# Kernel tuning notes

Measured on AMD Instinct MI355X. Metric: run time of the kernel, lower is better.

The kernel has to match this reference:

```python
import jax, jax.numpy as jnp
import numpy as np

D = 1024; DI = 2048; DS = 16; DTR = 64; K = 4          # mamba dims
HR = 16; DHR = 64                                       # rwkv heads
HA = 32; DHA = 32                                       # attention heads
NM = 6; NR = 4; NT = 2                                  # layer counts
B = 2; L = 1024


def _rms(x, w):
    return x * jax.lax.rsqrt(jnp.mean(x * x, axis=-1, keepdims=True) + 1e-6) * w


def _dwconv(x, w, b):
    # causal depthwise conv over seq; x [B,L,DI], w [K,1,DI]
    xp = jnp.pad(x, ((0, 0), (K - 1, 0), (0, 0)))
    y = jax.lax.conv_general_dilated(xp, w, (1,), 'VALID',
        dimension_numbers=('NWC', 'WIO', 'NWC'), feature_group_count=DI)
    return y + b


def _selective_scan(u, delta, A, Bm, Cm):
    # u,delta [B,L,DI]; A [DI,DS]; Bm,Cm [B,L,DS]
    def step(h, inp):
        u_t, d_t, b_t, c_t = inp
        dA = jnp.exp(d_t[:, :, None] * A)                     # [B,DI,DS]
        h = h * dA + (d_t * u_t)[:, :, None] * b_t[:, None, :]
        return h, jnp.einsum('bds,bs->bd', h, c_t)
    h0 = jnp.zeros((u.shape[0], DI, DS), u.dtype)
    tm = lambda a: jnp.swapaxes(a, 0, 1)                      # time-major
    _, ys = jax.lax.scan(step, h0, (tm(u), tm(delta), tm(Bm), tm(Cm)))
    return jnp.swapaxes(ys, 0, 1)


def _mamba(x, p):
    norm, Win, cw, cb, Wx, Wdt, bdt, Alog, Dp, Wout = p
    xn = _rms(x, norm)
    xz = xn @ Win                                             # [B,L,2*DI]
    xc, z = jnp.split(xz, 2, axis=-1)
    xc = jax.nn.silu(_dwconv(xc, cw, cb))
    xdbl = xc @ Wx                                            # [B,L,DTR+2*DS]
    dt = xdbl[..., :DTR]
    Bm = xdbl[..., DTR:DTR + DS]
    Cm = xdbl[..., DTR + DS:]
    delta = jax.nn.softplus(dt @ Wdt + bdt)                   # [B,L,DI]
    A = -jnp.exp(Alog)
    y = _selective_scan(xc, delta, A, Bm, Cm) + Dp * xc
    y = y * jax.nn.silu(z)
    return x + y @ Wout


def _rwkv(x, p):
    norm, mu, Wr, Wk, Wv, Wo, wlog, u = p
    Bb, Ll = x.shape[0], x.shape[1]
    xn = _rms(x, norm)
    xs = jnp.pad(xn, ((0, 0), (1, 0), (0, 0)))[:, :-1, :]     # token shift
    mix = lambda m: xn * m + xs * (1.0 - m)
    r = (mix(mu[0]) @ Wr).reshape(Bb, Ll, HR, DHR)
    k = (mix(mu[1]) @ Wk).reshape(Bb, Ll, HR, DHR)
    v = (mix(mu[2]) @ Wv).reshape(Bb, Ll, HR, DHR)
    w = jnp.exp(-jnp.exp(wlog))                               # decay in (0,1)
    def step(S, inp):
        r_t, k_t, v_t = inp                                   # [B,HR,DHR]
        kv = jnp.einsum('bhk,bhv->bhkv', k_t, v_t)
        y = jnp.einsum('bhk,bhkv->bhv', r_t, S + u[None, :, :, None] * kv)
        return w[None, :, :, None] * S + kv, y
    S0 = jnp.zeros((Bb, HR, DHR, DHR), x.dtype)
    tm = lambda a: jnp.swapaxes(a, 0, 1)
    _, ys = jax.lax.scan(step, S0, (tm(r), tm(k), tm(v)))
    y = jnp.swapaxes(ys, 0, 1).reshape(Bb, Ll, D)
    return x + y @ Wo


def _mha(x, p):
    Wq, bq, Wk, bk, Wv, bv, Wo, bo = p
    q = jnp.einsum('bld,dhk->blhk', x, Wq) + bq
    k = jnp.einsum('bld,dhk->blhk', x, Wk) + bk
    v = jnp.einsum('bld,dhk->blhk', x, Wv) + bv
    scale = 1.0 / float(np.sqrt(DHA))
    att = jax.nn.softmax(jnp.einsum('blhk,bmhk->bhlm', q, k) * scale, axis=-1)
    o = jnp.einsum('bhlm,bmhk->blhk', att, v)
    return jnp.einsum('blhk,hkd->bld', o, Wo) + bo


def setup_inputs() -> dict:
    key = jax.random.key(0)
    ks = iter(jax.random.split(key, 40))
    nrm = lambda s, sc=0.02: jax.random.normal(next(ks), s, jnp.float32) * sc
    return {
        'x': jax.random.normal(next(ks), (B, L, D), jnp.float32),
        'm_norm': jnp.ones((NM, D), jnp.float32),
        'm_Win': nrm((NM, D, 2 * DI)),
        'm_conv_w': nrm((NM, K, 1, DI)),
        'm_conv_b': jnp.zeros((NM, DI), jnp.float32),
        'm_Wx': nrm((NM, DI, DTR + 2 * DS)),
        'm_Wdt': nrm((NM, DTR, DI)),
        'm_bdt': jnp.full((NM, DI), -4.6, jnp.float32),
        'm_Alog': jnp.broadcast_to(jnp.log(jnp.arange(1, DS + 1, dtype=jnp.float32)), (NM, DI, DS)) + jnp.zeros((NM, DI, DS), jnp.float32),
        'm_D': jnp.ones((NM, DI), jnp.float32),
        'm_Wout': nrm((NM, DI, D)),
        'r_norm': jnp.ones((NR, D), jnp.float32),
        'r_mu': jax.random.uniform(next(ks), (NR, 3, D), jnp.float32),
        'r_Wr': nrm((NR, D, D)), 'r_Wk': nrm((NR, D, D)),
        'r_Wv': nrm((NR, D, D)), 'r_Wo': nrm((NR, D, D)),
        'r_wlog': nrm((NR, HR, DHR), 0.5),
        'r_u': nrm((NR, HR, DHR), 0.5),
        'a_Wq': nrm((NT, D, HA, DHA)), 'a_bq': jnp.zeros((NT, HA, DHA), jnp.float32),
        'a_Wk': nrm((NT, D, HA, DHA)), 'a_bk': jnp.zeros((NT, HA, DHA), jnp.float32),
        'a_Wv': nrm((NT, D, HA, DHA)), 'a_bv': jnp.zeros((NT, HA, DHA), jnp.float32),
        'a_Wo': nrm((NT, HA, DHA, D)), 'a_bo': jnp.zeros((NT, D), jnp.float32),
        'f_W': nrm((3 * D, 3)), 'f_b': jnp.zeros((3,), jnp.float32),
    }


def reference(x, m_norm, m_Win, m_conv_w, m_conv_b, m_Wx, m_Wdt, m_bdt, m_Alog, m_D, m_Wout,
              r_norm, r_mu, r_Wr, r_Wk, r_Wv, r_Wo, r_wlog, r_u,
              a_Wq, a_bq, a_Wk, a_bk, a_Wv, a_bv, a_Wo, a_bo, f_W, f_b):
    m = x
    for i in range(NM):
        m = _mamba(m, (m_norm[i], m_Win[i], m_conv_w[i], m_conv_b[i], m_Wx[i],
                       m_Wdt[i], m_bdt[i], m_Alog[i], m_D[i], m_Wout[i]))
    r = x
    for i in range(NR):
        r = _rwkv(r, (r_norm[i], r_mu[i], r_Wr[i], r_Wk[i], r_Wv[i], r_Wo[i],
                      r_wlog[i], r_u[i]))
    t = x
    for i in range(NT):
        t = _mha(t, (a_Wq[i], a_bq[i], a_Wk[i], a_bk[i], a_Wv[i], a_bv[i],
                     a_Wo[i], a_bo[i]))
    combined = jnp.concatenate([m, r, t], axis=-1)           # [B,L,3*D]
    return jax.nn.softmax(combined @ f_W + f_b, axis=-1)     # [B,L,3]
```

## Files before the change

### kernel.cpp

```cpp
#include <hip/hip_runtime.h>
#include <hip/hip_bf16.h>
#include <cstddef>

#define D_   1024
#define DI_  2048
#define DS_  16
#define DTR_ 64
#define KC_  4
#define HR_  16
#define DHR_ 64
#define HA_  32
#define DHA_ 32
#define NM_  6
#define NR_  4
#define NT_  2
#define B_   2
#define L_   1024
#define NBL  (B_*L_)

typedef __hip_bfloat16 bf16;
typedef __attribute__((ext_vector_type(8))) short short8v;
typedef __attribute__((ext_vector_type(4))) float float4v;

__device__ __forceinline__ float bfbits2f(unsigned short u) {
    return __uint_as_float(((unsigned int)u) << 16);
}
__device__ __forceinline__ float b2f(bf16 x) { return __bfloat162float(x); }
__device__ __forceinline__ unsigned short f2bfbits(float f) {
    bf16 h = __float2bfloat16(f);
    return *reinterpret_cast<unsigned short*>(&h);
}
__device__ __forceinline__ float ldf(const void* p, long i, int bf) {
    if (bf) return bfbits2f(((const unsigned short*)p)[i]);
    return ((const float*)p)[i];
}
__device__ __forceinline__ float softplus_f(float x) {
    return x > 20.f ? x : log1pf(__expf(x));
}
__device__ __forceinline__ float silu_f(float x) {
    return x / (1.f + __expf(-x));
}

__global__ __launch_bounds__(256) void diag_k(float* __restrict__ out, float code)
{
    const int idx = blockIdx.x * 256 + threadIdx.x;
    if (idx < NBL * 3) out[idx] = (idx == 0 ? code : 0.f);
}

__global__ __launch_bounds__(64) void detect_k(const void* __restrict__ x,
                                               int* __restrict__ flag)
{
    const unsigned short* u = (const unsigned short*)x;
    int local = 0;
    for (int i = threadIdx.x; i < 1024; i += 64) {
        const float av = fabsf(bfbits2f(u[i]));
        if (!(av < 1e6f)) local = 1;
    }
    const unsigned long long b = __ballot(local);
    if (threadIdx.x == 0) flag[0] = b ? 0 : 1;
}

#define BM 64
#define BN 64
#define TK 64
#define LDT 72

__global__ __launch_bounds__(256) void gemm_k(
    const void* __restrict__ A, int lda, int aDt,
    const void* __restrict__ W, long woff,
    const void* __restrict__ bias, long boff, int hasBias,
    void* __restrict__ C, int ldc, int cDt,
    int N, int K, int act, int acc,
    const int* __restrict__ flagp)
{
    const int bf = *flagp;
    __shared__ short As[BM * LDT];
    __shared__ short Bs[BN * LDT];
    const int bm = blockIdx.y * BM;
    const int bn = blockIdx.x * BN;
    const int tid = threadIdx.x;
    const int lane = tid & 63;
    const int wid = tid >> 6;
    const int wr = wid >> 1, wc = wid & 1;

    const int sa_row = tid >> 2;
    const int sa_kq  = (tid & 3) << 4;
    const int sb_col = tid & 63;
    const int sb_kq  = (tid >> 6) << 4;
    const int sb_gn  = bn + sb_col;

    float4v accv[2][2] = {};

    for (int k0 = 0; k0 < K; k0 += TK) {
        {
            short8v a0, a1;
            const size_t aoff = (size_t)(bm + sa_row) * lda + k0 + sa_kq;
            if (aDt) {
                a0 = *(const short8v*)((const unsigned short*)A + aoff);
                a1 = *(const short8v*)((const unsigned short*)A + aoff + 8);
            } else {
                const float* ap = (const float*)A + aoff;
                const float4 v0 = *(const float4*)(ap + 0);
                const float4 v1 = *(const float4*)(ap + 4);
                const float4 v2 = *(const float4*)(ap + 8);
                const float4 v3 = *(const float4*)(ap + 12);
                a0[0]=f2bfbits(v0.x); a0[1]=f2bfbits(v0.y); a0[2]=f2bfbits(v0.z); a0[3]=f2bfbits(v0.w);
                a0[4]=f2bfbits(v1.x); a0[5]=f2bfbits(v1.y); a0[6]=f2bfbits(v1.z); a0[7]=f2bfbits(v1.w);
                a1[0]=f2bfbits(v2.x); a1[1]=f2bfbits(v2.y); a1[2]=f2bfbits(v2.z); a1[3]=f2bfbits(v2.w);
                a1[4]=f2bfbits(v3.x); a1[5]=f2bfbits(v3.y); a1[6]=f2bfbits(v3.z); a1[7]=f2bfbits(v3.w);
            }
            *(short8v*)&As[sa_row * LDT + sa_kq + 0] = a0;
            *(short8v*)&As[sa_row * LDT + sa_kq + 8] = a1;
        }
        {
            short8v b0, b1;
            #pragma unroll
            for (int j = 0; j < 8; ++j) { b0[j] = 0; b1[j] = 0; }
            if (sb_gn < N) {
                const long wbase = woff + (long)(k0 + sb_kq) * N + sb_gn;
                if (bf) {
                    const unsigned short* wp = (const unsigned short*)W;
                    #pragma unroll
                    for (int j = 0; j < 8; ++j) {
                        b0[j] = (short)wp[wbase + (long)j * N];
                        b1[j] = (short)wp[wbase + (long)(j + 8) * N];
                    }
                } else {
                    const float* wp = (const float*)W;
                    #pragma unroll
                    for (int j = 0; j < 8; ++j) {
                        b0[j] = (short)f2bfbits(wp[wbase + (long)j * N]);
                        b1[j] = (short)f2bfbits(wp[wbase + (long)(j + 8) * N]);
                    }
                }
            }
            *(short8v*)&Bs[sb_col * LDT + sb_kq + 0] = b0;
            *(short8v*)&Bs[sb_col * LDT + sb_kq + 8] = b1;
        }
        __syncthreads();
        {
            const int r  = lane & 15;
            const int kb = (lane >> 4) << 3;
            #pragma unroll
            for (int ks = 0; ks < TK; ks += 32) {
                const int kg = ks + kb;
                const short8v a0 = *(const short8v*)&As[(wr*32 +      r) * LDT + kg];
                const short8v a1 = *(const short8v*)&As[(wr*32 + 16 + r) * LDT + kg];
                const short8v b0 = *(const short8v*)&Bs[(wc*32 +      r) * LDT + kg];
                const short8v b1 = *(const short8v*)&Bs[(wc*32 + 16 + r) * LDT + kg];
                accv[0][0] = __builtin_amdgcn_mfma_f32_16x16x32_bf16(a0, b0, accv[0][0], 0, 0, 0);
                accv[0][1] = __builtin_amdgcn_mfma_f32_16x16x32_bf16(a0, b1, accv[0][1], 0, 0, 0);
                accv[1][0] = __builtin_amdgcn_mfma_f32_16x16x32_bf16(a1, b0, accv[1][0], 0, 0, 0);
                accv[1][1] = __builtin_amdgcn_mfma_f32_16x16x32_bf16(a1, b1, accv[1][1], 0, 0, 0);
            }
        }
        __syncthreads();
    }

    const int crow0 = bm + wr * 32 + ((lane >> 4) << 2);
    const int ccol0 = bn + wc * 32 + (lane & 15);
    #pragma unroll
    for (int ni = 0; ni < 2; ++ni) {
        const int col = ccol0 + ni * 16;
        if (col < N) {
            const float bsv = hasBias ? ldf(bias, boff + col, bf) : 0.f;
            #pragma unroll
            for (int mi = 0; mi < 2; ++mi) {
                #pragma unroll
                for (int j = 0; j < 4; ++j) {
                    const int row = crow0 + mi * 16 + j;
                    float r = accv[mi][ni][j] + bsv;
                    if (act == 1) r = softplus_f(r);
                    if (cDt) {
                        ((bf16*)C)[(size_t)row * ldc + col] = __float2bfloat16(r);
                    } else {
                        float* cp = (float*)C + (size_t)row * ldc + col;
                        if (acc) r += *cp;
                        *cp = r;
                    }
                }
            }
        }
    }
}

__global__ __launch_bounds__(256) void cast3_k(const void* __restrict__ x,
    float* __restrict__ a, float* __restrict__ b, float* __restrict__ c,
    const int* __restrict__ flagp)
{
    const int bf = *flagp;
    const int idx = blockIdx.x * 256 + threadIdx.x;
    const float v = ldf(x, idx, bf);
    a[idx] = v; b[idx] = v; c[idx] = v;
}

__global__ __launch_bounds__(256) void rmsnorm_k(const float* __restrict__ x,
    const void* __restrict__ wgt, long woff, float* __restrict__ out,
    const int* __restrict__ flagp)
{
    const int bf = *flagp;
    const int row = blockIdx.x;
    const float* xr = x + (size_t)row * D_;
    float ss = 0.f;
    for (int i = threadIdx.x; i < D_; i += 256) { const float v = xr[i]; ss = fmaf(v, v, ss); }
    #pragma unroll
    for (int msk = 1; msk < 64; msk <<= 1) ss += __shfl_xor(ss, msk);
    __shared__ float red[4];
    if ((threadIdx.x & 63) == 0) red[threadIdx.x >> 6] = ss;
    __syncthreads();
    ss = red[0] + red[1] + red[2] + red[3];
    const float scale = rsqrtf(ss * (1.f / D_) + 1e-6f);
    float* orow = out + (size_t)row * D_;
    for (int i = threadIdx.x; i < D_; i += 256)
        orow[i] = xr[i] * scale * ldf(wgt, woff + i, bf);
}

__global__ __launch_bounds__(256) void conv_silu_k(const bf16* __restrict__ xz,
    const void* __restrict__ cw, long cwoff, const void* __restrict__ cb, long cboff,
    bf16* __restrict__ out, const int* __restrict__ flagp)
{
    const int bf = *flagp;
    const int idx = blockIdx.x * 256 + threadIdx.x;
    const int c = idx & (DI_ - 1);
    const int l = (idx >> 11) & (L_ - 1);
    const int b = idx >> 21;
    float acc = ldf(cb, cboff + c, bf);
    #pragma unroll
    for (int j = 0; j < KC_; ++j) {
        const int ls = l - (KC_ - 1) + j;
        if (ls >= 0)
            acc = fmaf(b2f(xz[((size_t)(b * L_ + ls)) * (2 * DI_) + c]),
                       ldf(cw, cwoff + j * DI_ + c, bf), acc);
    }
    out[idx] = __float2bfloat16(silu_f(acc));
}

#define MS_NCH 16
#define MS_CH  (L_ / MS_NCH)

__global__ __launch_bounds__(256) void mamba_scan_k(
    const bf16* __restrict__ u, const bf16* __restrict__ dlt,
    const float* __restrict__ xdbl, bf16* __restrict__ xz,
    const void* __restrict__ Alog, long aoff, const void* __restrict__ Dp, long doff,
    const int* __restrict__ flagp)
{
    const int bf = *flagp;
    const int bid = blockIdx.x;
    const int d = bid & (DI_ - 1);
    const int b = bid >> 11;
    const int s = threadIdx.x & (DS_ - 1);
    const int c = threadIdx.x >> 4;
    const float Av = -__expf(ldf(Alog, aoff + d * DS_ + s, bf));
    const float Dv = ldf(Dp, doff + d, bf);

    __shared__ float Pl[MS_NCH][DS_];
    __shared__ float Sl[MS_NCH][DS_];

    const int l0 = c * MS_CH;

    float P = 1.f, S = 0.f;
    for (int i = 0; i < MS_CH; ++i) {
        const size_t row = (size_t)(b * L_ + l0 + i);
        const float ut = b2f(u[row * DI_ + d]);
        const float dt = b2f(dlt[row * DI_ + d]);
        const float Bv = xdbl[row * 96 + 64 + s];
        const float dA = __expf(dt * Av);
        P *= dA;
        S = fmaf(S, dA, dt * ut * Bv);
    }
    Pl[c][s] = P; Sl[c][s] = S;
    __syncthreads();

    float hs = 0.f;
    for (int cc = 0; cc < c; ++cc) hs = fmaf(hs, Pl[cc][s], Sl[cc][s]);

    for (int i = 0; i < MS_CH; ++i) {
        const size_t row = (size_t)(b * L_ + l0 + i);
        const float ut = b2f(u[row * DI_ + d]);
        const float dt = b2f(dlt[row * DI_ + d]);
        const float Bv = xdbl[row * 96 + 64 + s];
        const float Cv = xdbl[row * 96 + 80 + s];
        const float dA = __expf(dt * Av);
        hs = fmaf(hs, dA, dt * ut * Bv);
        float yp = hs * Cv;
        yp += __shfl_xor(yp, 1, 16);
        yp += __shfl_xor(yp, 2, 16);
        yp += __shfl_xor(yp, 4, 16);
        yp += __shfl_xor(yp, 8, 16);
        if (s == 0) {
            const float z = b2f(xz[row * (2 * DI_) + DI_ + d]);
            xz[row * (2 * DI_) + d] = __float2bfloat16((yp + Dv * ut) * silu_f(z));
        }
    }
}

__global__ __launch_bounds__(256) void rwkv_mix_k(const float* __restrict__ xn,
    const void* __restrict__ mu, long muoff, bf16* __restrict__ o0,
    bf16* __restrict__ o1, bf16* __restrict__ o2, const int* __restrict__ flagp)
{
    const int bf = *flagp;
    const int idx = blockIdx.x * 256 + threadIdx.x;
    const int d = idx & (D_ - 1);
    const int l = (idx >> 10) & (L_ - 1);
    const float cur = xn[idx];
    const float prev = (l > 0) ? xn[idx - D_] : 0.f;
    const float m0 = ldf(mu, muoff + d, bf);
    const float m1 = ldf(mu, muoff + D_ + d, bf);
    const float m2 = ldf(mu, muoff + 2 * D_ + d, bf);
    o0[idx] = __float2bfloat16(cur * m0 + prev * (1.f - m0));
    o1[idx] = __float2bfloat16(cur * m1 + prev * (1.f - m1));
    o2[idx] = __float2bfloat16(cur * m2 + prev * (1.f - m2));
}

#define RW_NCH 16
#define RW_CH  (L_ / RW_NCH)

__global__ __launch_bounds__(1024) void rwkv_scan_k(const bf16* __restrict__ R,
    const bf16* __restrict__ Kb, const bf16* __restrict__ V,
    const void* __restrict__ wlog, long woff, const void* __restrict__ uu, long uoff,
    bf16* __restrict__ Y, const int* __restrict__ flagp)
{
    const int bf = *flagp;
    const int bid = blockIdx.x;
    const int v = bid & (DHR_ - 1);
    const int h = (bid >> 6) & (HR_ - 1);
    const int b = bid >> 10;
    const int k = threadIdx.x & 63;
    const int c = threadIdx.x >> 6;
    const float ew = __expf(ldf(wlog, woff + h * DHR_ + k, bf));
    const float w  = __expf(-ew);
    const float wC = __expf(-ew * (float)RW_CH);
    const float uv = ldf(uu, uoff + h * DHR_ + k, bf);

    __shared__ float Se[RW_NCH][64];

    const int l0 = c * RW_CH;

    float S = 0.f;
    for (int i = 0; i < RW_CH; ++i) {
        const size_t off = ((size_t)(b * L_ + l0 + i)) * D_ + h * DHR_;
        const float kk = b2f(Kb[off + k]);
        const float vt = b2f(V[off + v]);
        S = fmaf(w, S, kk * vt);
    }
    Se[c][k] = S;
    __syncthreads();

    S = 0.f;
    for (int cc = 0; cc < c; ++cc) S = fmaf(wC, S, Se[cc][k]);

    for (int i = 0; i < RW_CH; ++i) {
        const size_t off = ((size_t)(b * L_ + l0 + i)) * D_ + h * DHR_;
        const float r  = b2f(R[off + k]);
        const float kk = b2f(Kb[off + k]);
        const float vt = b2f(V[off + v]);
        const float kv = kk * vt;
        float yp = r * fmaf(uv, kv, S);
        S = fmaf(w, S, kv);
        yp += __shfl_xor(yp, 1);
        yp += __shfl_xor(yp, 2);
        yp += __shfl_xor(yp, 4);
        yp += __shfl_xor(yp, 8);
        yp += __shfl_xor(yp, 16);
        yp += __shfl_xor(yp, 32);
        if (k == 0) Y[off + v] = __float2bfloat16(yp);
    }
}

__global__ __launch_bounds__(256) void mha_attn_k(const bf16* __restrict__ Q,
    const bf16* __restrict__ Kx, const bf16* __restrict__ V, bf16* __restrict__ O)
{
    const int b = blockIdx.z, h = blockIdx.y;
    const int ql = blockIdx.x * 256 + threadIdx.x;
    __shared__ float Ks[32][33];
    __shared__ float Vs[32][33];
    float q[32], o[32];
    #pragma unroll
    for (int d = 0; d < 32; ++d) o[d] = 0.f;
    float mrun = -1e30f, lsum = 0.f;
    const size_t qoff = ((size_t)(b * L_ + ql)) * D_ + h * DHA_;
    #pragma unroll
    for (int d = 0; d < 32; ++d) q[d] = b2f(Q[qoff + d]) * 0.1767766952966369f;

    for (int kt = 0; kt < L_; kt += 32) {
        __syncthreads();
        {
            const int r = threadIdx.x >> 3;
            const int c = (threadIdx.x & 7) << 2;
            const size_t koff = ((size_t)(b * L_ + kt + r)) * D_ + h * DHA_ + c;
            const ushort4 k4 = *(const ushort4*)((const unsigned short*)Kx + koff);
            Ks[r][c + 0] = bfbits2f(k4.x); Ks[r][c + 1] = bfbits2f(k4.y);
            Ks[r][c + 2] = bfbits2f(k4.z); Ks[r][c + 3] = bfbits2f(k4.w);
            const ushort4 v4 = *(const ushort4*)((const unsigned short*)V + koff);
            Vs[r][c + 0] = bfbits2f(v4.x); Vs[r][c + 1] = bfbits2f(v4.y);
            Vs[r][c + 2] = bfbits2f(v4.z); Vs[r][c + 3] = bfbits2f(v4.w);
        }
        __syncthreads();
        for (int j = 0; j < 32; ++j) {
            float s = 0.f;
            #pragma unroll
            for (int d = 0; d < 32; ++d) s = fmaf(q[d], Ks[j][d], s);
            const float mn = fmaxf(mrun, s);
            const float corr = __expf(mrun - mn);
            const float p = __expf(s - mn);
            lsum = lsum * corr + p;
            #pragma unroll
            for (int d = 0; d < 32; ++d) o[d] = o[d] * corr + p * Vs[j][d];
            mrun = mn;
        }
    }
    const float inv = 1.f / lsum;
    #pragma unroll
    for (int d = 0; d < 32; ++d) O[qoff + d] = __float2bfloat16(o[d] * inv);
}

__global__ __launch_bounds__(256) void final_k(const float* __restrict__ m,
    const float* __restrict__ r, const float* __restrict__ t,
    const void* __restrict__ fW, const void* __restrict__ fb,
    float* __restrict__ out, const int* __restrict__ flagp)
{
    const int bf = *flagp;
    const int row = blockIdx.x;
    float p0 = 0.f, p1 = 0.f, p2 = 0.f;
    for (int i = threadIdx.x; i < 3 * D_; i += 256) {
        float v;
        if (i < D_)          v = m[(size_t)row * D_ + i];
        else if (i < 2 * D_) v = r[(size_t)row * D_ + i - D_];
        else                 v = t[(size_t)row * D_ + i - 2 * D_];
        p0 = fmaf(v, ldf(fW, (long)i * 3 + 0, bf), p0);
        p1 = fmaf(v, ldf(fW, (long)i * 3 + 1, bf), p1);
        p2 = fmaf(v, ldf(fW, (long)i * 3 + 2, bf), p2);
    }
    #pragma unroll
    for (int msk = 1; msk < 64; msk <<= 1) {
        p0 += __shfl_xor(p0, msk);
        p1 += __shfl_xor(p1, msk);
        p2 += __shfl_xor(p2, msk);
    }
    __shared__ float red[4][3];
    if ((threadIdx.x & 63) == 0) {
        const int w = threadIdx.x >> 6;
        red[w][0] = p0; red[w][1] = p1; red[w][2] = p2;
    }
    __syncthreads();
    if (threadIdx.x == 0) {
        const float l0 = red[0][0] + red[1][0] + red[2][0] + red[3][0] + ldf(fb, 0, bf);
        const float l1 = red[0][1] + red[1][1] + red[2][1] + red[3][1] + ldf(fb, 1, bf);
        const float l2 = red[0][2] + red[1][2] + red[2][2] + red[3][2] + ldf(fb, 2, bf);
        const float mx = fmaxf(l0, fmaxf(l1, l2));
        const float e0 = __expf(l0 - mx), e1 = __expf(l1 - mx), e2 = __expf(l2 - mx);
        const float inv = 1.f / (e0 + e1 + e2);
        out[row * 3 + 0] = e0 * inv;
        out[row * 3 + 1] = e1 * inv;
        out[row * 3 + 2] = e2 * inv;
    }
}

extern "C" void kernel_launch(void* const* d_in, const int* in_sizes, int n_in,
                              void* d_out, int out_size, void* d_ws, size_t ws_size,
                              hipStream_t stream)
{
    float* out = (float*)d_out;

    static const int expected[29] = {
        2097152, 6144, 25165824, 49152, 12288, 1179648, 786432, 12288,
        196608, 12288, 12582912, 4096, 12288, 4194304, 4194304, 4194304,
        4194304, 4096, 4096, 2097152, 2048, 2097152, 2048, 2097152, 2048,
        2097152, 2048, 9216, 3 };
    int bad = (n_in == 29) ? -1 : 29;
    if (bad < 0)
        for (int i = 0; i < 29; ++i)
            if (in_sizes[i] != expected[i]) { bad = i; break; }
    if (bad >= 0) {
        diag_k<<<24, 256, 0, stream>>>(out, 1000.f + 8.f * bad);
        return;
    }

    const size_t REQ = 64 + 3ull * 8388608 + 8388608 + 16777216 + 8388608 + 786432;
    if (ws_size < REQ) {
        diag_k<<<24, 256, 0, stream>>>(out, 2048.f + (float)(ws_size >> 20));
        return;
    }
    char* base = (char*)d_ws;
    int*   flag = (int*)base;
    float* resM = (float*)(base + 64);
    float* resR = resM + 2097152;
    float* resT = resR + 2097152;
    float* bufN = resT + 2097152;
    bf16*  XZ16 = (bf16*)(bufN + 2097152);
    bf16*  U16  = XZ16 + (size_t)NBL * 4096;
    float* XD   = (float*)(U16 + (size_t)NBL * 2048);

    bf16* q0 = XZ16;
    bf16* q1 = XZ16 + 1 * 2097152;
    bf16* q2 = XZ16 + 2 * 2097152;
    bf16* q3 = XZ16 + 3 * 2097152;
    bf16* u0 = U16;
    bf16* u1 = U16 + 2097152;

    const void* x        = d_in[0];
    const void* m_norm   = d_in[1];
    const void* m_Win    = d_in[2];
    const void* m_conv_w = d_in[3];
    const void* m_conv_b = d_in[4];
    const void* m_Wx     = d_in[5];
    const void* m_Wdt    = d_in[6];
    const void* m_bdt    = d_in[7];
    const void* m_Alog   = d_in[8];
    const void* m_D      = d_in[9];
    const void* m_Wout   = d_in[10];
    const void* r_norm   = d_in[11];
    const void* r_mu     = d_in[12];
    const void* r_Wr     = d_in[13];
    const void* r_Wk     = d_in[14];
    const void* r_Wv     = d_in[15];
    const void* r_Wo     = d_in[16];
    const void* r_wlog   = d_in[17];
    const void* r_u      = d_in[18];
    const void* a_Wq     = d_in[19];
    const void* a_bq     = d_in[20];
    const void* a_Wk     = d_in[21];
    const void* a_bk     = d_in[22];
    const void* a_Wv     = d_in[23];
    const void* a_bv     = d_in[24];
    const void* a_Wo     = d_in[25];
    const void* a_bo     = d_in[26];
    const void* f_W      = d_in[27];
    const void* f_b      = d_in[28];

    auto gemm = [&](const void* A, int lda, int aDt, const void* W, long woff,
                    const void* bias, long boff, int hasBias,
                    void* C, int ldc, int cDt, int N, int K, int act, int acc) {
        dim3 g((N + BN - 1) / BN, NBL / BM);
        gemm_k<<<g, 256, 0, stream>>>(A, lda, aDt, W, woff, bias, boff, hasBias,
                                      C, ldc, cDt, N, K, act, acc, flag);
    };

    detect_k<<<1, 64, 0, stream>>>(x, flag);
    cast3_k<<<8192, 256, 0, stream>>>(x, resM, resR, resT, flag);

    for (int i = 0; i < NM_; ++i) {
        rmsnorm_k<<<NBL, 256, 0, stream>>>(resM, m_norm, (long)i * D_, bufN, flag);
        gemm(bufN, D_, 0, m_Win, (long)i * D_ * 2 * DI_, nullptr, 0, 0,
             XZ16, 2 * DI_, 1, 2 * DI_, D_, 0, 0);
        conv_silu_k<<<16384, 256, 0, stream>>>(XZ16, m_conv_w, (long)i * KC_ * DI_,
                                               m_conv_b, (long)i * DI_, U16, flag);
        gemm(U16, DI_, 1, m_Wx, (long)i * DI_ * 96, nullptr, 0, 0,
             XD, 96, 0, 96, DI_, 0, 0);
        gemm(XD, 96, 0, m_Wdt, (long)i * DTR_ * DI_, m_bdt, (long)i * DI_, 1,
             bufN, DI_, 1, DI_, DTR_, 1 , 0);
        mamba_scan_k<<<B_ * DI_, 256, 0, stream>>>(U16, (const bf16*)bufN, XD, XZ16,
            m_Alog, (long)i * DI_ * DS_, m_D, (long)i * DI_, flag);
        gemm(XZ16, 2 * DI_, 1, m_Wout, (long)i * DI_ * D_, nullptr, 0, 0,
             resM, D_, 0, D_, DI_, 0, 1 );
    }

    for (int i = 0; i < NR_; ++i) {
        rmsnorm_k<<<NBL, 256, 0, stream>>>(resR, r_norm, (long)i * D_, bufN, flag);
        rwkv_mix_k<<<8192, 256, 0, stream>>>(bufN, r_mu, (long)i * 3 * D_,
                                             q0, q1, q2, flag);
        gemm(q0, D_, 1, r_Wr, (long)i * D_ * D_, nullptr, 0, 0, u0, D_, 1, D_, D_, 0, 0);
        gemm(q1, D_, 1, r_Wk, (long)i * D_ * D_, nullptr, 0, 0, u1, D_, 1, D_, D_, 0, 0);
        gemm(q2, D_, 1, r_Wv, (long)i * D_ * D_, nullptr, 0, 0, q3, D_, 1, D_, D_, 0, 0);
        rwkv_scan_k<<<B_ * HR_ * DHR_, RW_NCH * 64, 0, stream>>>(u0, u1, q3,
            r_wlog, (long)i * HR_ * DHR_, r_u, (long)i * HR_ * DHR_, q0, flag);
        gemm(q0, D_, 1, r_Wo, (long)i * D_ * D_, nullptr, 0, 0, resR, D_, 0, D_, D_, 0, 1);
    }

    for (int i = 0; i < NT_; ++i) {
        gemm(resT, D_, 0, a_Wq, (long)i * D_ * HA_ * DHA_, a_bq, (long)i * HA_ * DHA_, 1,
             u0, D_, 1, D_, D_, 0, 0);
        gemm(resT, D_, 0, a_Wk, (long)i * D_ * HA_ * DHA_, a_bk, (long)i * HA_ * DHA_, 1,
             u1, D_, 1, D_, D_, 0, 0);
        gemm(resT, D_, 0, a_Wv, (long)i * D_ * HA_ * DHA_, a_bv, (long)i * HA_ * DHA_, 1,
             q3, D_, 1, D_, D_, 0, 0);
        mha_attn_k<<<dim3(L_ / 256, HA_, B_), 256, 0, stream>>>(u0, u1, q3, q0);
        gemm(q0, D_, 1, a_Wo, (long)i * HA_ * DHA_ * D_, a_bo, (long)i * D_, 1,
             resT, D_, 0, D_, HA_ * DHA_, 0, 0 );
    }

    final_k<<<NBL, 256, 0, stream>>>(resM, resR, resT, f_W, f_b, out, flag);
}
```

Measured before the change: 4.958 ms.

## Rewrite MHA attention as flash-attention using bf16 MFMA tiles

Replaces the scalar per-thread online-softmax attention with a flash-attention style kernel. Each wave computes QK^T and PV for 16 queries using 16x16x32 bf16 MFMA instructions. K and V are staged as bf16 in LDS, with V transposed, and softmax probabilities go through a per-wave LDS buffer. The grid grows to 64 queries per block, which raises parallelism. Probabilities are rounded to bf16 before the PV product, which slightly changes numerics.

```diff
diff --git a/kernel.cpp b/kernel.cpp
--- a/kernel.cpp
+++ b/kernel.cpp
@@ -367,51 +367,99 @@
     }
 }
 
+#define LDK 40
+#define LDV 72
+
 __global__ __launch_bounds__(256) void mha_attn_k(const bf16* __restrict__ Q,
     const bf16* __restrict__ Kx, const bf16* __restrict__ V, bf16* __restrict__ O)
 {
     const int b = blockIdx.z, h = blockIdx.y;
-    const int ql = blockIdx.x * 256 + threadIdx.x;
-    __shared__ float Ks[32][33];
-    __shared__ float Vs[32][33];
-    float q[32], o[32];
-    #pragma unroll
-    for (int d = 0; d < 32; ++d) o[d] = 0.f;
-    float mrun = -1e30f, lsum = 0.f;
-    const size_t qoff = ((size_t)(b * L_ + ql)) * D_ + h * DHA_;
-    #pragma unroll
-    for (int d = 0; d < 32; ++d) q[d] = b2f(Q[qoff + d]) * 0.1767766952966369f;
-
-    for (int kt = 0; kt < L_; kt += 32) {
+    const int qt = blockIdx.x;
+    const int tid = threadIdx.x;
+    const int lane = tid & 63;
+    const int wid = tid >> 6;
+
+    __shared__ __align__(16) short Ks[64 * LDK];
+    __shared__ __align__(16) short Vt[32 * LDV];
+    __shared__ __align__(16) short Ps[4][16 * LDV];
+
+    const int fc  = lane & 15;
+    const int g   = lane >> 4;
+    const int fk8 = g << 3;
+
+    const int q0 = qt * 64 + wid * 16;
+
+    const size_t qoff = ((size_t)(b * L_ + q0 + fc)) * D_ + h * DHA_ + fk8;
+    const short8v qf = *(const short8v*)((const unsigned short*)Q + qoff);
+
+    float4v o0 = {}, o1 = {};
+    float m[4] = {-1e30f, -1e30f, -1e30f, -1e30f};
+    float l[4] = {0.f, 0.f, 0.f, 0.f};
+    const float scale = 0.1767766952966369f;
+
+    const int sr = tid >> 2;
+    const int sc = (tid & 3) << 3;
+
+    for (int kt = 0; kt < L_; kt += 64) {
         __syncthreads();
         {
-            const int r = threadIdx.x >> 3;
-            const int c = (threadIdx.x & 7) << 2;
-            const size_t koff = ((size_t)(b * L_ + kt + r)) * D_ + h * DHA_ + c;
-            const ushort4 k4 = *(const ushort4*)((const unsigned short*)Kx + koff);
-            Ks[r][c + 0] = bfbits2f(k4.x); Ks[r][c + 1] = bfbits2f(k4.y);
-            Ks[r][c + 2] = bfbits2f(k4.z); Ks[r][c + 3] = bfbits2f(k4.w);
-            const ushort4 v4 = *(const ushort4*)((const unsigned short*)V + koff);
-            Vs[r][c + 0] = bfbits2f(v4.x); Vs[r][c + 1] = bfbits2f(v4.y);
-            Vs[r][c + 2] = bfbits2f(v4.z); Vs[r][c + 3] = bfbits2f(v4.w);
+            const size_t koff = ((size_t)(b * L_ + kt + sr)) * D_ + h * DHA_ + sc;
+            const short8v k8 = *(const short8v*)((const unsigned short*)Kx + koff);
+            *(short8v*)&Ks[sr * LDK + sc] = k8;
+            const short8v v8 = *(const short8v*)((const unsigned short*)V + koff);
+            #pragma unroll
+            for (int j = 0; j < 8; ++j)
+                Vt[(sc + j) * LDV + sr] = v8[j];
         }
         __syncthreads();
-        for (int j = 0; j < 32; ++j) {
-            float s = 0.f;
+
+        float4v sv[4];
+        #pragma unroll
+        for (int nt = 0; nt < 4; ++nt) {
+            const short8v kf = *(const short8v*)&Ks[(nt * 16 + fc) * LDK + fk8];
+            float4v z = {};
+            sv[nt] = __builtin_amdgcn_mfma_f32_16x16x32_bf16(qf, kf, z, 0, 0, 0);
+        }
+
+        #pragma unroll
+        for (int j = 0; j < 4; ++j) {
+            float mt = fmaxf(fmaxf(sv[0][j], sv[1][j]), fmaxf(sv[2][j], sv[3][j])) * scale;
             #pragma unroll
-            for (int d = 0; d < 32; ++d) s = fmaf(q[d], Ks[j][d], s);
-            const float mn = fmaxf(mrun, s);
-            const float corr = __expf(mrun - mn);
-            const float p = __expf(s - mn);
-            lsum = lsum * corr + p;
+            for (int msk = 1; msk < 16; msk <<= 1) mt = fmaxf(mt, __shfl_xor(mt, msk));
+            const float mn = fmaxf(m[j], mt);
+            const float corr = __expf(m[j] - mn);
+            m[j] = mn;
+            float sum = 0.f;
             #pragma unroll
-            for (int d = 0; d < 32; ++d) o[d] = o[d] * corr + p * Vs[j][d];
-            mrun = mn;
-        }
-    }
-    const float inv = 1.f / lsum;
+            for (int nt = 0; nt < 4; ++nt) {
+                const float p = __expf(fmaf(sv[nt][j], scale, -mn));
+                sum += p;
+                Ps[wid][(g * 4 + j) * LDV + nt * 16 + fc] = (short)f2bfbits(p);
+            }
+            #pragma unroll
+            for (int msk = 1; msk < 16; msk <<= 1) sum += __shfl_xor(sum, msk);
+            l[j] = l[j] * corr + sum;
+            o0[j] *= corr;
+            o1[j] *= corr;
+        }
+
+        #pragma unroll
+        for (int kc = 0; kc < 2; ++kc) {
+            const short8v pf = *(const short8v*)&Ps[wid][fc * LDV + kc * 32 + fk8];
+            const short8v v0 = *(const short8v*)&Vt[(fc) * LDV + kc * 32 + fk8];
+            const short8v v1 = *(const short8v*)&Vt[(16 + fc) * LDV + kc * 32 + fk8];
+            o0 = __builtin_amdgcn_mfma_f32_16x16x32_bf16(pf, v0, o0, 0, 0, 0);
+            o1 = __builtin_amdgcn_mfma_f32_16x16x32_bf16(pf, v1, o1, 0, 0, 0);
+        }
+    }
+
     #pragma unroll
-    for (int d = 0; d < 32; ++d) O[qoff + d] = __float2bfloat16(o[d] * inv);
+    for (int j = 0; j < 4; ++j) {
+        const float inv = 1.f / l[j];
+        const size_t ooff = ((size_t)(b * L_ + q0 + g * 4 + j)) * D_ + h * DHA_;
+        O[ooff + fc]      = __float2bfloat16(o0[j] * inv);
+        O[ooff + 16 + fc] = __float2bfloat16(o1[j] * inv);
+    }
 }
 
 __global__ __launch_bounds__(256) void final_k(const float* __restrict__ m,
@@ -574,7 +622,7 @@
              u1, D_, 1, D_, D_, 0, 0);
         gemm(resT, D_, 0, a_Wv, (long)i * D_ * HA_ * DHA_, a_bv, (long)i * HA_ * DHA_, 1,
              q3, D_, 1, D_, D_, 0, 0);
-        mha_attn_k<<<dim3(L_ / 256, HA_, B_), 256, 0, stream>>>(u0, u1, q3, q0);
+        mha_attn_k<<<dim3(L_ / 64, HA_, B_), 256, 0, stream>>>(u0, u1, q3, q0);
         gemm(q0, D_, 1, a_Wo, (long)i * HA_ * DHA_ * D_, a_bo, (long)i * D_, 1,
              resT, D_, 0, D_, HA_ * DHA_, 0, 0 );
     }
```

Result: faster. 4.168 ms (-15.9%).
